# Optimization experiments

Hardware: AMD Instinct MI355X
Metric: run time of the kernel (lower is better)

Reference implementation:

```python
import jax, jax.numpy as jnp
import numpy as np

NUM_STATES = 1_000_000
VOCAB = 1024
ARCS_PER_STATE = 10   # arcs per non-start state
MAX_ORDER = 4         # max backoff-chain length
BATCH = 1024


def _build_lm(seed=0):
    """Synthetic but structurally valid n-gram WFST suffix tree (numpy, vectorized)."""
    rng = np.random.default_rng(seed)
    N, V, K = NUM_STATES, VOCAB, ARCS_PER_STATE
    num_arcs = V + (N - 1) * K

    # start state (0): one arc per vocab label (UNK fallback guarantees full coverage)
    start_ilabels = np.arange(V, dtype=np.int32)
    start_to = rng.integers(0, N, size=V, dtype=np.int32)
    # other states: K strictly-increasing labels each (sorted by ilabel, as in _init_from_suffix_tree)
    lab = np.sort(rng.integers(0, V - K + 1, size=(N - 1, K)), axis=1).astype(np.int32)
    lab = lab + np.arange(K, dtype=np.int32)[None, :]
    other_to = rng.integers(0, N, size=(N - 1) * K, dtype=np.int32)

    ilabels = np.concatenate([start_ilabels, lab.reshape(-1)])
    to_states = np.concatenate([start_to, other_to])
    from_states = np.concatenate([
        np.zeros(V, dtype=np.int32),
        np.repeat(np.arange(1, N, dtype=np.int32), K),
    ])
    arcs_weights = (-rng.uniform(0.1, 10.0, size=num_arcs)).astype(np.float32)

    # state metadata: arc ranges, orders, backoff targets
    state_start_arcs = np.concatenate([[0], V + np.arange(N - 1, dtype=np.int64) * K]).astype(np.int32)
    state_end_arcs = state_start_arcs + np.concatenate([[V], np.full(N - 1, K, dtype=np.int64)]).astype(np.int32)

    # order blocks: state 0 -> order 1; [1, n2] order 2; (n2, n3] order 3; rest order 4
    n2 = 1 + int(0.6 * (N - 1))
    n3 = n2 + int(0.3 * (N - 1))
    state_order = np.full(N, 4, dtype=np.int32)
    state_order[0] = 1
    state_order[1:n2 + 1] = 2
    state_order[n2 + 1:n3 + 1] = 3
    backoff_to_states = np.zeros(N, dtype=np.int32)          # order-2 states back off to start
    backoff_to_states[n2 + 1:n3 + 1] = rng.integers(1, n2 + 1, size=n3 - n2, dtype=np.int32)
    backoff_to_states[n3 + 1:] = rng.integers(n2 + 1, n3 + 1, size=N - 1 - n3, dtype=np.int32)
    backoff_weights = (-rng.uniform(0.1, 5.0, size=N)).astype(np.float32)
    backoff_weights[0] = 0.0

    return dict(
        arcs_weights=jnp.asarray(arcs_weights),
        backoff_weights=jnp.asarray(backoff_weights),
        from_states=jnp.asarray(from_states),
        to_states=jnp.asarray(to_states),
        ilabels=jnp.asarray(ilabels),
        backoff_to_states=jnp.asarray(backoff_to_states),
        state_start_arcs=jnp.asarray(state_start_arcs),
        state_end_arcs=jnp.asarray(state_end_arcs),
        state_order=jnp.asarray(state_order),
    )


def setup_inputs() -> dict:
    inp = _build_lm(seed=0)
    key = jax.random.key(0)
    inp["states"] = jax.random.randint(key, (BATCH,), 0, NUM_STATES, dtype=jnp.int32)
    return inp


def reference(arcs_weights, backoff_weights, from_states, to_states, ilabels,
              backoff_to_states, state_start_arcs, state_end_arcs, state_order, states):
    """Batched LM advance: for each state and every vocab label, follow backoff
    chain until an arc with that ilabel is found; return (scores[B,V], next_states[B,V])."""
    V = VOCAB
    num_arcs = ilabels.shape[0]
    # arcs are globally sorted by (from_state, ilabel) -> single sorted key array
    keys = from_states.astype(jnp.int32) * V + ilabels.astype(jnp.int32)  # max ~1.02e9, fits int32

    B = states.shape[0]
    labels = jnp.arange(V, dtype=jnp.int32)[None, :]            # [1,V]
    cur = jnp.broadcast_to(states[:, None], (B, V))              # [B,V]
    score = jnp.zeros((B, V), dtype=arcs_weights.dtype)
    nxt = jnp.zeros((B, V), dtype=jnp.int32)
    done = jnp.zeros((B, V), dtype=bool)

    for _ in range(MAX_ORDER):  # backoff depth bounded by max n-gram order
        q = cur * V + labels                                     # [B,V] query keys
        pos = jnp.clip(jnp.searchsorted(keys, q), 0, num_arcs - 1)
        found = (keys[pos] == q) & (~done)
        score = score + jnp.where(found, arcs_weights[pos], jnp.zeros((), arcs_weights.dtype))
        nxt = jnp.where(found, to_states[pos], nxt)
        backoff = (~done) & (~found)
        score = score + jnp.where(backoff, backoff_weights[cur], jnp.zeros((), arcs_weights.dtype))
        cur = jnp.where(backoff, backoff_to_states[cur], cur)
        done = done | found
    return score, nxt
```

## Files before the change

kernel.cpp:

```cpp
#include <hip/hip_runtime.h>

#define VOCAB 1024
#define MAXC  4
#define MAXK  16

__global__ __launch_bounds__(256)
void ngram_advance(const float* __restrict__ arcs_weights,
                   const float* __restrict__ backoff_weights,
                   const int*   __restrict__ to_states,
                   const int*   __restrict__ ilabels,
                   const int*   __restrict__ backoff_to_states,
                   const int*   __restrict__ state_start_arcs,
                   const int*   __restrict__ state_end_arcs,
                   const int*   __restrict__ states,
                   float* __restrict__ out_scores,
                   float* __restrict__ out_next)
{
    __shared__ int   ch_state[MAXC];
    __shared__ int   ch_sa[MAXC];
    __shared__ int   ch_na[MAXC];
    __shared__ float ch_bw[MAXC];
    __shared__ int   ch_len;
    __shared__ int   s_lab[MAXC][MAXK];
    __shared__ float s_wt [MAXC][MAXK];
    __shared__ int   s_to [MAXC][MAXK];

    const int b   = blockIdx.x;
    const int tid = threadIdx.x;

    if (tid == 0) {
        int cur = states[b];
        int len = 0;
        for (;;) {
            int sa = state_start_arcs[cur];
            ch_state[len] = cur;
            ch_sa[len]    = sa;
            ch_na[len]    = state_end_arcs[cur] - sa;
            ch_bw[len]    = backoff_weights[cur];
            ++len;
            if (cur == 0 || len == MAXC) break;
            cur = backoff_to_states[cur];
        }
        ch_len = len;
    }
    __syncthreads();

    const int len = ch_len;

    for (int idx = tid; idx < MAXC * MAXK; idx += blockDim.x) {
        int l = idx / MAXK, j = idx % MAXK;
        if (l < len && ch_state[l] != 0 && j < ch_na[l]) {
            int a = ch_sa[l] + j;
            s_lab[l][j] = ilabels[a];
            s_wt [l][j] = arcs_weights[a];
            s_to [l][j] = to_states[a];
        }
    }
    __syncthreads();

    const long long obase = (long long)b * VOCAB;
    for (int v = tid; v < VOCAB; v += blockDim.x) {
        float score = 0.f;
        int   nxt   = 0;
        bool  done  = false;
        for (int l = 0; l < len && !done; ++l) {
            if (ch_state[l] == 0) {
                int a = ch_sa[l] + v;
                score += arcs_weights[a];
                nxt    = to_states[a];
                done   = true;
            } else {
                int  na    = ch_na[l];
                bool found = false;
                for (int j = 0; j < na; ++j) {
                    if (s_lab[l][j] == v) {
                        score += s_wt[l][j];
                        nxt    = s_to[l][j];
                        found  = true;
                    }
                }
                if (found) done = true;
                else       score += ch_bw[l];
            }
        }
        out_scores[obase + v] = score;
        out_next[obase + v]   = (float)nxt;
    }
}

extern "C" void kernel_launch(void* const* d_in, const int* in_sizes, int n_in,
                              void* d_out, int out_size, void* d_ws, size_t ws_size,
                              hipStream_t stream) {
    const float* arcs_weights    = (const float*)d_in[0];
    const float* backoff_weights = (const float*)d_in[1];
    const int*   to_states       = (const int*)d_in[3];
    const int*   ilabels         = (const int*)d_in[4];
    const int*   backoff_to      = (const int*)d_in[5];
    const int*   ssa             = (const int*)d_in[6];
    const int*   sea             = (const int*)d_in[7];
    const int*   states          = (const int*)d_in[9];
    const int B = in_sizes[9];

    float* out_scores = (float*)d_out;
    float* out_next   = out_scores + (size_t)B * VOCAB;

    ngram_advance<<<dim3(B), dim3(256), 0, stream>>>(
        arcs_weights, backoff_weights, to_states, ilabels, backoff_to,
        ssa, sea, states, out_scores, out_next);
}
```

Baseline: 168.5 us.

## Replace per-vocab arc scan with shared-memory label lookup table built via atomicMin

```diff
diff --git a/kernel.cpp b/kernel.cpp
--- a/kernel.cpp
+++ b/kernel.cpp
@@ -2,7 +2,7 @@
 
 #define VOCAB 1024
 #define MAXC  4
-#define MAXK  16
+#define SLOT_SHIFT 8
 
 __global__ __launch_bounds__(256)
 void ngram_advance(const float* __restrict__ arcs_weights,
@@ -16,27 +16,29 @@
                    float* __restrict__ out_scores,
                    float* __restrict__ out_next)
 {
-    __shared__ int   ch_state[MAXC];
-    __shared__ int   ch_sa[MAXC];
-    __shared__ int   ch_na[MAXC];
-    __shared__ float ch_bw[MAXC];
+    __shared__ int   tab[VOCAB];
+    __shared__ float s_wt[64];
+    __shared__ int   s_to[64];
+    __shared__ int   ch_state[MAXC], ch_sa[MAXC], ch_na[MAXC];
+    __shared__ float ch_bwsum[MAXC];
     __shared__ int   ch_len;
-    __shared__ int   s_lab[MAXC][MAXK];
-    __shared__ float s_wt [MAXC][MAXK];
-    __shared__ int   s_to [MAXC][MAXK];
 
     const int b   = blockIdx.x;
     const int tid = threadIdx.x;
 
+    for (int v = tid; v < VOCAB; v += 256) tab[v] = 0x7FFFFFFF;
+
     if (tid == 0) {
         int cur = states[b];
         int len = 0;
+        float acc = 0.f;
         for (;;) {
             int sa = state_start_arcs[cur];
             ch_state[len] = cur;
             ch_sa[len]    = sa;
             ch_na[len]    = state_end_arcs[cur] - sa;
-            ch_bw[len]    = backoff_weights[cur];
+            ch_bwsum[len] = acc;
+            acc += backoff_weights[cur];
             ++len;
             if (cur == 0 || len == MAXC) break;
             cur = backoff_to_states[cur];
@@ -47,44 +49,36 @@
 
     const int len = ch_len;
 
-    for (int idx = tid; idx < MAXC * MAXK; idx += blockDim.x) {
-        int l = idx / MAXK, j = idx % MAXK;
+    if (tid < 64) {
+        int l = tid >> 4, j = tid & 15;
         if (l < len && ch_state[l] != 0 && j < ch_na[l]) {
             int a = ch_sa[l] + j;
-            s_lab[l][j] = ilabels[a];
-            s_wt [l][j] = arcs_weights[a];
-            s_to [l][j] = to_states[a];
+            s_wt[tid] = arcs_weights[a];
+            s_to[tid] = to_states[a];
+            atomicMin(&tab[ilabels[a]], (l << SLOT_SHIFT) | tid);
         }
     }
     __syncthreads();
 
-    const long long obase = (long long)b * VOCAB;
-    for (int v = tid; v < VOCAB; v += blockDim.x) {
-        float score = 0.f;
-        int   nxt   = 0;
-        bool  done  = false;
-        for (int l = 0; l < len && !done; ++l) {
-            if (ch_state[l] == 0) {
-                int a = ch_sa[l] + v;
-                score += arcs_weights[a];
-                nxt    = to_states[a];
-                done   = true;
-            } else {
-                int  na    = ch_na[l];
-                bool found = false;
-                for (int j = 0; j < na; ++j) {
-                    if (s_lab[l][j] == v) {
-                        score += s_wt[l][j];
-                        nxt    = s_to[l][j];
-                        found  = true;
-                    }
-                }
-                if (found) done = true;
-                else       score += ch_bw[l];
-            }
+    const int    last   = len - 1;
+    const float  bwlast = ch_bwsum[last];
+    const int    sa0    = ch_sa[last];
+    const size_t obase  = (size_t)b * VOCAB;
+    for (int v = tid; v < VOCAB; v += 256) {
+        int   t  = tab[v];
+        int   fl = t >> SLOT_SHIFT;
+        float sc;
+        int   nx;
+        if (fl < last) {
+            int slot = t & 255;
+            sc = ch_bwsum[fl] + s_wt[slot];
+            nx = s_to[slot];
+        } else {
+            sc = bwlast + arcs_weights[sa0 + v];
+            nx = to_states[sa0 + v];
         }
-        out_scores[obase + v] = score;
-        out_next[obase + v]   = (float)nxt;
+        out_scores[obase + v] = sc;
+        out_next[obase + v]   = (float)nx;
     }
 }
 
```

Measured after the change: 156.9 us. 1.07x faster.
